# Kernel tuning notes

Measured on AMD Instinct MI355X. Metric: run time of the kernel, lower is better.

The kernel has to match this reference:

```python
import jax, jax.numpy as jnp
import numpy as np

N, E, IN, HID, H, C, L, G = 20000, 640000, 128, 256, 8, 32, 5, 64
NEG_SLOPE = 0.2


def _layernorm(x, g, b, eps=1e-5):
    mu = jnp.mean(x, axis=-1, keepdims=True)
    var = jnp.mean((x - mu) ** 2, axis=-1, keepdims=True)
    return (x - mu) * jax.lax.rsqrt(var + eps) * g + b


def _gatv2(h, src, dst, Wl, bl, Wr, br, att, out_bias):
    # h: [N, HID]; src/dst: [E+N] (self loops appended)
    n = h.shape[0]
    xl = (h @ Wl + bl).reshape(n, H, C)  # source transform
    xr = (h @ Wr + br).reshape(n, H, C)  # target transform
    e = jax.nn.leaky_relu(xl[src] + xr[dst], NEG_SLOPE)       # [Etot, H, C]
    logits = jnp.einsum('ehc,hc->eh', e, att)                  # [Etot, H]
    m = jax.ops.segment_max(logits, dst, num_segments=n)       # segment softmax over dst
    a = jnp.exp(logits - m[dst])
    s = jax.ops.segment_sum(a, dst, num_segments=n)
    alpha = a / (s[dst] + 1e-16)                               # [Etot, H]
    out = jax.ops.segment_sum(alpha[:, :, None] * xl[src], dst, num_segments=n)
    return out.reshape(n, HID) + out_bias


def setup_inputs() -> dict:
    key = jax.random.key(0)
    ks = jax.random.split(key, 16)
    sc = 0.05
    inp = {
        'x': jax.random.normal(ks[0], (N, IN), jnp.float32),
        'edge_index': jax.random.randint(ks[1], (2, E), 0, N, jnp.int64),
        'batch': jnp.sort(jax.random.randint(ks[2], (N,), 0, G, jnp.int64)),
        'proj_W': jax.random.normal(ks[3], (IN, HID), jnp.float32) * sc,
        'proj_b': jnp.zeros((HID,), jnp.float32),
        'Wl': jax.random.normal(ks[4], (L, HID, HID), jnp.float32) * sc,
        'bl': jnp.zeros((L, HID), jnp.float32),
        'Wr': jax.random.normal(ks[5], (L, HID, HID), jnp.float32) * sc,
        'br': jnp.zeros((L, HID), jnp.float32),
        'att': jax.random.normal(ks[6], (L, H, C), jnp.float32) * sc,
        'out_bias': jnp.zeros((L, HID), jnp.float32),
        'ln_g': jnp.ones((L, HID), jnp.float32),
        'ln_b': jnp.zeros((L, HID), jnp.float32),
    }
    return inp


def reference(x, edge_index, batch, proj_W, proj_b, Wl, bl, Wr, br, att, out_bias, ln_g, ln_b):
    n = x.shape[0]
    loops = jnp.arange(n, dtype=edge_index.dtype)
    src = jnp.concatenate([edge_index[0], loops])  # add_self_loops=True
    dst = jnp.concatenate([edge_index[1], loops])
    h = x @ proj_W + proj_b
    for i in range(L):  # dropout = identity in eval mode
        conv = _gatv2(h, src, dst, Wl[i], bl[i], Wr[i], br[i], att[i], out_bias[i])
        h = _layernorm(h + jax.nn.elu(conv), ln_g[i], ln_b[i])
    counts = jax.ops.segment_sum(jnp.ones((n,), h.dtype), batch, num_segments=G)
    gsum = jax.ops.segment_sum(h, batch, num_segments=G)
    graph_emb = gsum / jnp.maximum(counts, 1.0)[:, None]  # global_mean_pool
    return graph_emb, h, batch
```

## Files before the change

kernel.cpp:

```cpp
#include <hip/hip_runtime.h>
#include <hip/hip_bf16.h>

#define NN   20000
#define NE   640000
#define INF_ 128
#define HID  256
#define NL   5
#define NG   64

typedef __hip_bfloat16 bf16;
typedef __attribute__((ext_vector_type(4))) float f32x4;
typedef __attribute__((ext_vector_type(8))) short bf16x8;

#if __has_builtin(__builtin_amdgcn_exp2f)
#define EXP2F __builtin_amdgcn_exp2f
#else
#define EXP2F exp2f
#endif

__device__ __forceinline__ float b2f(bf16 v) { return __bfloat162float(v); }
__device__ __forceinline__ short f2bs(float v) {
  union { bf16 h; short s; } u; u.h = __float2bfloat16(v); return u.s;
}

#if __has_builtin(__builtin_amdgcn_update_dpp)
template<int CTRL>
__device__ __forceinline__ float dpp_add(float v) {
  int t = __builtin_amdgcn_update_dpp(0, __float_as_int(v), CTRL, 0xF, 0xF, true);
  return v + __int_as_float(t);
}
__device__ __forceinline__ float hsum8(float v) {
  v = dpp_add<0xB1>(v);
  v = dpp_add<0x4E>(v);
  v = dpp_add<0x141>(v);
  return v;
}
__device__ __forceinline__ float wsum64(float v) {
  v = hsum8(v);
  v = dpp_add<0x140>(v);
  v += __shfl_xor(v, 16);
  v += __shfl_xor(v, 32);
  return v;
}
#else
__device__ __forceinline__ float hsum8(float v) {
  v += __shfl_xor(v, 1);  v += __shfl_xor(v, 2);  v += __shfl_xor(v, 4);
  return v;
}
__device__ __forceinline__ float wsum64(float v) {
  v += __shfl_xor(v, 1);  v += __shfl_xor(v, 2);  v += __shfl_xor(v, 4);
  v += __shfl_xor(v, 8);  v += __shfl_xor(v, 16); v += __shfl_xor(v, 32);
  return v;
}
#endif

__global__ void detect_kernel(const int* __restrict__ ei,
                              const int* __restrict__ batch,
                              int* __restrict__ flags) {
  if (blockIdx.x == 0) {
    const int k = threadIdx.x;
    const bool e_bad = (k < 40) && (ei[2 * (k * 15999) + 1] != 0);
    const bool b_bad = (k < 40) && (batch[2 * (k * 249) + 1] != 0);
    const int e64 = __any(e_bad) ? 0 : 1;
    const int b64 = __any(b_bad) ? 0 : 1;
    if (k == 0) { flags[0] = e64; flags[1] = b64; }
  }
}

__device__ __forceinline__ int ld_i(const int* p, int f, size_t idx) {
  return f ? p[2 * idx] : p[idx];
}

__global__ void hist_kernel(const int* __restrict__ ei, const int* __restrict__ flags,
                            int* __restrict__ deg) {
  int e = blockIdx.x * blockDim.x + threadIdx.x;
  if (e >= NE) return;
  int f = flags[0];
  int d = ld_i(ei, f, (size_t)NE + e);
  if ((unsigned)d < NN) atomicAdd(&deg[d], 1);
}

#define SCAN_NB ((NN + 255) / 256)
__global__ __launch_bounds__(256) void scan1_kernel(
    const int* __restrict__ deg, int* __restrict__ off, int* __restrict__ bsum)
{
  __shared__ int sh[256];
  const int t = threadIdx.x;
  const int i = blockIdx.x * 256 + t;
  const int v = (i < NN) ? deg[i] : 0;
  sh[t] = v;
  __syncthreads();
  for (int d = 1; d < 256; d <<= 1) {
    int nv = (t >= d) ? sh[t - d] : 0;
    __syncthreads();
    sh[t] += nv;
    __syncthreads();
  }
  if (i < NN) off[i] = sh[t] - v;
  if (t == 255) bsum[blockIdx.x] = sh[255];
}

__global__ __launch_bounds__(128) void scan2_kernel(
    const int* __restrict__ bsum, int* __restrict__ boff, int* __restrict__ off)
{
  __shared__ int sh[128];
  const int t = threadIdx.x;
  const int v = (t < SCAN_NB) ? bsum[t] : 0;
  sh[t] = v;
  __syncthreads();
  for (int d = 1; d < 128; d <<= 1) {
    int nv = (t >= d) ? sh[t - d] : 0;
    __syncthreads();
    sh[t] += nv;
    __syncthreads();
  }
  if (t < SCAN_NB) boff[t] = sh[t] - v;
  if (t == SCAN_NB - 1) off[NN] = sh[t];
}

__global__ __launch_bounds__(256) void scan3_kernel(
    int* __restrict__ off, const int* __restrict__ boff, int* __restrict__ tmp)
{
  const int i = blockIdx.x * 256 + threadIdx.x;
  if (i < NN) {
    const int val = off[i] + boff[blockIdx.x];
    off[i] = val;
    tmp[i] = val;
  }
}

__global__ void scatter_kernel(const int* __restrict__ ei, const int* __restrict__ flags,
                               int* __restrict__ tmp, int* __restrict__ csr) {
  int e = blockIdx.x * blockDim.x + threadIdx.x;
  if (e >= NE) return;
  int f = flags[0];
  int d = ld_i(ei, f, (size_t)NE + e);
  int s = ld_i(ei, f, (size_t)e);
  if ((unsigned)d < NN) {
    int p = atomicAdd(&tmp[d], 1);
    int sv = ((unsigned)s < NN) ? s : 0;
    if ((unsigned)p < NE) csr[p] = sv * (HID * 2);
  }
}

__global__ __launch_bounds__(256) void prep_btf_kernel(
    const float* __restrict__ Wl, const float* __restrict__ Wr,
    short* __restrict__ BTl, short* __restrict__ BTr)
{
  const int z = blockIdx.y;
  const float* src = (z < NL) ? Wl + (size_t)z * HID * HID
                              : Wr + (size_t)(z - NL) * HID * HID;
  short* dst = (z < NL) ? BTl + (size_t)z * HID * HID
                        : BTr + (size_t)(z - NL) * HID * HID;
  const int g = blockIdx.x * 256 + threadIdx.x;
  const int ln   = g & 63;
  const int frag = (g >> 6) & 63;
  const int half = g >> 12;
  const int nf = frag >> 3, kk = frag & 7;
  const int n  = half * 128 + nf * 16 + (ln & 15);
  const int k0 = kk * 32 + (ln >> 4) * 8;
  bf16x8 outv;
#pragma unroll
  for (int j = 0; j < 8; ++j) outv[j] = f2bs(src[(size_t)(k0 + j) * HID + n]);
  *(bf16x8*)&dst[(size_t)g * 8] = outv;
}

template<int K, bool A_BF16>
__global__ __launch_bounds__(256) void gemm_bias_kernel(
    const void* __restrict__ Av, const float* __restrict__ B,
    const float* __restrict__ bias, float* __restrict__ Cf,
    bf16* __restrict__ Cb, int M)
{
  constexpr int N = 256;
  constexpr int LDB = K + 8;
  __shared__ __align__(16) short bT[32 * LDB];
  const int tid = threadIdx.x;
  const int n0 = blockIdx.x * 32;
  const int m_base = blockIdx.y * 256;

  if (tid < K) {
    const float* brow = B + (size_t)tid * N + n0;
#pragma unroll
    for (int j = 0; j < 32; ++j) bT[j * LDB + tid] = f2bs(brow[j]);
  }
  __syncthreads();

  const int wave = tid >> 6;
  const int lane = tid & 63;
  const int r    = lane & 15;
  const int quad = lane >> 4;
  const int m_wave = m_base + wave * 64;

  f32x4 acc[4][2];
#pragma unroll
  for (int i = 0; i < 4; ++i) { acc[i][0] = (f32x4)0.0f; acc[i][1] = (f32x4)0.0f; }

#pragma unroll
  for (int kk = 0; kk < K / 32; ++kk) {
    const int kof = kk * 32 + quad * 8;
    bf16x8 b0 = *(const bf16x8*)&bT[r * LDB + kof];
    bf16x8 b1 = *(const bf16x8*)&bT[(r + 16) * LDB + kof];
#pragma unroll
    for (int sm = 0; sm < 4; ++sm) {
      const int row = m_wave + sm * 16 + r;
      bf16x8 a = (bf16x8)(short)0;
      if (row < M) {
        if constexpr (A_BF16) {
          a = *(const bf16x8*)((const short*)Av + (size_t)row * K + kof);
        } else {
          const float* ap = (const float*)Av + (size_t)row * K + kof;
          f32x4 lo = *(const f32x4*)ap;
          f32x4 hi = *(const f32x4*)(ap + 4);
#pragma unroll
          for (int j = 0; j < 4; ++j) { a[j] = f2bs(lo[j]); a[4 + j] = f2bs(hi[j]); }
        }
      }
      acc[sm][0] = __builtin_amdgcn_mfma_f32_16x16x32_bf16(a, b0, acc[sm][0], 0, 0, 0);
      acc[sm][1] = __builtin_amdgcn_mfma_f32_16x16x32_bf16(a, b1, acc[sm][1], 0, 0, 0);
    }
  }

  const float bv0 = bias[n0 + r];
  const float bv1 = bias[n0 + 16 + r];
#pragma unroll
  for (int sm = 0; sm < 4; ++sm) {
#pragma unroll
    for (int rg = 0; rg < 4; ++rg) {
      const int row = m_wave + sm * 16 + quad * 4 + rg;
      if (row < M) {
        size_t i0 = (size_t)row * N + n0 + r;
        float v0 = acc[sm][0][rg] + bv0;
        float v1 = acc[sm][1][rg] + bv1;
        if (Cf) { Cf[i0] = v0; Cf[i0 + 16] = v1; }
        if (Cb) {
          ((unsigned short*)Cb)[i0]      = (unsigned short)f2bs(v0);
          ((unsigned short*)Cb)[i0 + 16] = (unsigned short)f2bs(v1);
        }
      }
    }
  }
}

template<bool A_BF16>
__global__ __launch_bounds__(256) void gemm_dual_kernel(
    const void* __restrict__ Av,
    const float* __restrict__ Bl, const float* __restrict__ Br,
    const float* __restrict__ bl, const float* __restrict__ br,
    bf16* __restrict__ Cl, bf16* __restrict__ Cr, int M)
{
  constexpr int K = HID, N = 256;
  constexpr int LDB = K + 8;
  __shared__ __align__(16) short bTl[32 * LDB];
  __shared__ __align__(16) short bTr[32 * LDB];
  const int tid = threadIdx.x;
  const int n0 = blockIdx.x * 32;
  const int m_base = blockIdx.y * 256;

  {
    const float* browl = Bl + (size_t)tid * N + n0;
    const float* browr = Br + (size_t)tid * N + n0;
#pragma unroll
    for (int j = 0; j < 32; ++j) {
      bTl[j * LDB + tid] = f2bs(browl[j]);
      bTr[j * LDB + tid] = f2bs(browr[j]);
    }
  }
  __syncthreads();

  const int wave = tid >> 6;
  const int lane = tid & 63;
  const int r    = lane & 15;
  const int quad = lane >> 4;
  const int m_wave = m_base + wave * 64;

  f32x4 accl[4][2], accr[4][2];
#pragma unroll
  for (int i = 0; i < 4; ++i) {
    accl[i][0] = (f32x4)0.0f; accl[i][1] = (f32x4)0.0f;
    accr[i][0] = (f32x4)0.0f; accr[i][1] = (f32x4)0.0f;
  }

#pragma unroll
  for (int kk = 0; kk < K / 32; ++kk) {
    const int kof = kk * 32 + quad * 8;
    bf16x8 b0l = *(const bf16x8*)&bTl[r * LDB + kof];
    bf16x8 b1l = *(const bf16x8*)&bTl[(r + 16) * LDB + kof];
    bf16x8 b0r = *(const bf16x8*)&bTr[r * LDB + kof];
    bf16x8 b1r = *(const bf16x8*)&bTr[(r + 16) * LDB + kof];
#pragma unroll
    for (int sm = 0; sm < 4; ++sm) {
      const int row = m_wave + sm * 16 + r;
      bf16x8 a = (bf16x8)(short)0;
      if (row < M) {
        if constexpr (A_BF16) {
          a = *(const bf16x8*)((const short*)Av + (size_t)row * K + kof);
        } else {
          const float* ap = (const float*)Av + (size_t)row * K + kof;
          f32x4 lo = *(const f32x4*)ap;
          f32x4 hi = *(const f32x4*)(ap + 4);
#pragma unroll
          for (int j = 0; j < 4; ++j) { a[j] = f2bs(lo[j]); a[4 + j] = f2bs(hi[j]); }
        }
      }
      accl[sm][0] = __builtin_amdgcn_mfma_f32_16x16x32_bf16(a, b0l, accl[sm][0], 0, 0, 0);
      accl[sm][1] = __builtin_amdgcn_mfma_f32_16x16x32_bf16(a, b1l, accl[sm][1], 0, 0, 0);
      accr[sm][0] = __builtin_amdgcn_mfma_f32_16x16x32_bf16(a, b0r, accr[sm][0], 0, 0, 0);
      accr[sm][1] = __builtin_amdgcn_mfma_f32_16x16x32_bf16(a, b1r, accr[sm][1], 0, 0, 0);
    }
  }

  const float bl0v = bl[n0 + r],  bl1v = bl[n0 + 16 + r];
  const float br0v = br[n0 + r],  br1v = br[n0 + 16 + r];
#pragma unroll
  for (int sm = 0; sm < 4; ++sm) {
#pragma unroll
    for (int rg = 0; rg < 4; ++rg) {
      const int row = m_wave + sm * 16 + quad * 4 + rg;
      if (row < M) {
        size_t i0 = (size_t)row * N + n0 + r;
        ((unsigned short*)Cl)[i0]      = (unsigned short)f2bs(accl[sm][0][rg] + bl0v);
        ((unsigned short*)Cl)[i0 + 16] = (unsigned short)f2bs(accl[sm][1][rg] + bl1v);
        ((unsigned short*)Cr)[i0]      = (unsigned short)f2bs(accr[sm][0][rg] + br0v);
        ((unsigned short*)Cr)[i0 + 16] = (unsigned short)f2bs(accr[sm][1][rg] + br1v);
      }
    }
  }
}

__global__ __launch_bounds__(256) void gemm_dual_tiled_kernel(
    const short* __restrict__ Ab,
    const short* __restrict__ BTl, const short* __restrict__ BTr,
    const float* __restrict__ bl, const float* __restrict__ br,
    bf16* __restrict__ Cl, bf16* __restrict__ Cr, int M)
{
  constexpr int K = HID;
  __shared__ __align__(16) short bfr[32768];
  const int tid  = threadIdx.x;
  const int lane = tid & 63;
  const int wv   = tid >> 6;
  const int bx   = blockIdx.x;
  const int n0   = (bx & 1) * 128;
  const short* BTf = (bx < 2) ? BTl : BTr;
  const float* bias = (bx < 2) ? bl : br;
  bf16* C = (bx < 2) ? Cl : Cr;
  const short* src = BTf + (size_t)(bx & 1) * 32768;

#pragma unroll
  for (int it = 0; it < 16; ++it) {
    const int c = it * 256 + tid;
    *(bf16x8*)&bfr[(size_t)c * 8] = *(const bf16x8*)&src[(size_t)c * 8];
  }

  const int r    = lane & 15;
  const int quad = lane >> 4;
  const int m_wave = blockIdx.y * 128 + wv * 32;

  const int ar0 = min(m_wave + r, M - 1);
  const int ar1 = min(m_wave + 16 + r, M - 1);
  const short* a0p = Ab + (size_t)ar0 * K + quad * 8;
  const short* a1p = Ab + (size_t)ar1 * K + quad * 8;
  bf16x8 a0[8], a1[8];
#pragma unroll
  for (int kk = 0; kk < 8; ++kk) {
    a0[kk] = *(const bf16x8*)(a0p + kk * 32);
    a1[kk] = *(const bf16x8*)(a1p + kk * 32);
  }

  __syncthreads();

  f32x4 acc[2][8];
#pragma unroll
  for (int sm = 0; sm < 2; ++sm)
#pragma unroll
    for (int nf = 0; nf < 8; ++nf) acc[sm][nf] = (f32x4)0.0f;

#pragma unroll
  for (int kk = 0; kk < 8; ++kk) {
#pragma unroll
    for (int nf = 0; nf < 8; ++nf) {
      const bf16x8 b = *(const bf16x8*)&bfr[((nf * 8 + kk) * 64 + lane) * 8];
      acc[0][nf] = __builtin_amdgcn_mfma_f32_16x16x32_bf16(a0[kk], b, acc[0][nf], 0, 0, 0);
      acc[1][nf] = __builtin_amdgcn_mfma_f32_16x16x32_bf16(a1[kk], b, acc[1][nf], 0, 0, 0);
    }
  }

  float bv[8];
#pragma unroll
  for (int nf = 0; nf < 8; ++nf) bv[nf] = bias[n0 + nf * 16 + r];

#pragma unroll
  for (int sm = 0; sm < 2; ++sm) {
#pragma unroll
    for (int rg = 0; rg < 4; ++rg) {
      const int row = m_wave + sm * 16 + quad * 4 + rg;
      if (row < M) {
        unsigned short* cp = (unsigned short*)C + (size_t)row * 256 + n0 + r;
#pragma unroll
        for (int nf = 0; nf < 8; ++nf)
          cp[nf * 16] = (unsigned short)f2bs(acc[sm][nf][rg] + bv[nf]);
      }
    }
  }
}

__global__ __launch_bounds__(256) void gat_layer_kernel(
    const bf16* __restrict__ xl, const bf16* __restrict__ xr,
    float* __restrict__ h, bf16* __restrict__ h_bf,
    const int* __restrict__ off, const int* __restrict__ csr,
    const float* __restrict__ att, const float* __restrict__ outb,
    const float* __restrict__ lng, const float* __restrict__ lnb)
{
  const int lane = threadIdx.x & 63;
  const int node = __builtin_amdgcn_readfirstlane(blockIdx.x * 4 + (threadIdx.x >> 6));
  const int cb   = ((lane >> 3) << 5) + ((lane & 7) << 2);
  const unsigned cb2  = (unsigned)cb * 2;
  const unsigned selfo = (unsigned)node * (HID * 2) + cb2;
  const size_t base = (size_t)node * HID + cb;
  const char* xlc = (const char*)xl;

  const uint2 uxr = *(const uint2*)((const char*)xr + selfo);
  const uint2 uxl = *(const uint2*)(xlc + selfo);
  f32x4 xrv, xls;
  xrv[0] = __uint_as_float(uxr.x << 16); xrv[1] = __uint_as_float(uxr.x & 0xffff0000u);
  xrv[2] = __uint_as_float(uxr.y << 16); xrv[3] = __uint_as_float(uxr.y & 0xffff0000u);
  xls[0] = __uint_as_float(uxl.x << 16); xls[1] = __uint_as_float(uxl.x & 0xffff0000u);
  xls[2] = __uint_as_float(uxl.y << 16); xls[3] = __uint_as_float(uxl.y & 0xffff0000u);

  const f32x4 av = *(const f32x4*)(att + cb);
  f32x4 a6, a4;
#pragma unroll
  for (int c = 0; c < 4; ++c) {
    a6[c] = av[c] * (0.6f * 1.44269504f);
    a4[c] = av[c] * (0.4f * 1.44269504f);
  }

  const f32x4 ob = *(const f32x4*)(outb + cb);
  const f32x4 hv = *(const f32x4*)(h + base);
  const f32x4 g4 = *(const f32x4*)(lng + cb);
  const f32x4 b4 = *(const f32x4*)(lnb + cb);

  float pa = 0.f;
#pragma unroll
  for (int c = 0; c < 4; ++c) {
    float z = xls[c] + xrv[c];
    pa = fmaf(a6[c], z, pa);
    pa = fmaf(a4[c], fabsf(z), pa);
  }
  const float es = EXP2F(hsum8(pa));
  float s = es;
  f32x4 o;
#pragma unroll
  for (int c = 0; c < 4; ++c) o[c] = es * xls[c];

  int beg = __builtin_amdgcn_readfirstlane(off[node]);
  int end = __builtin_amdgcn_readfirstlane(off[node + 1]);
  if (beg < 0) beg = 0;
  if (end > NE) end = NE;
  const unsigned* csrb = (const unsigned*)csr;

  const int nblk = (end > beg) ? ((end - beg) >> 3) : 0;

  unsigned adr[8];
  uint2 bufA[8], bufB[8];

  auto LOADADR = [&](int blk) {
    const int pp = beg + blk * 8;
#pragma unroll
    for (int j = 0; j < 8; ++j) adr[j] = csrb[pp + j];
  };
  auto GATHER = [&](uint2 (&buf)[8]) {
#pragma unroll
    for (int j = 0; j < 8; ++j) buf[j] = *(const uint2*)(xlc + (adr[j] + cb2));
  };
  auto COMPUTE = [&](const uint2 (&buf)[8]) {
    f32x4 xv[8];
#pragma unroll
    for (int j = 0; j < 8; ++j) {
      xv[j][0] = __uint_as_float(buf[j].x << 16);
      xv[j][1] = __uint_as_float(buf[j].x & 0xffff0000u);
      xv[j][2] = __uint_as_float(buf[j].y << 16);
      xv[j][3] = __uint_as_float(buf[j].y & 0xffff0000u);
    }
    float e[8];
#pragma unroll
    for (int j = 0; j < 8; ++j) {
      float acc = 0.f;
#pragma unroll
      for (int c = 0; c < 4; ++c) {
        float z = xv[j][c] + xrv[c];
        acc = fmaf(a6[c], z, acc);
        acc = fmaf(a4[c], fabsf(z), acc);
      }
      e[j] = EXP2F(hsum8(acc));
    }
    s += (((e[0] + e[1]) + (e[2] + e[3])) + ((e[4] + e[5]) + (e[6] + e[7])));
#pragma unroll
    for (int c = 0; c < 4; ++c) {
      float c0 = fmaf(e[0], xv[0][c], fmaf(e[1], xv[1][c],
                 fmaf(e[2], xv[2][c], fmaf(e[3], xv[3][c], o[c]))));
      float c1 = fmaf(e[4], xv[4][c], fmaf(e[5], xv[5][c],
                 fmaf(e[6], xv[6][c], e[7] * xv[7][c])));
      o[c] = c0 + c1;
    }
  };

  if (nblk > 0) {
    LOADADR(0);
    GATHER(bufA);
    if (nblk > 1) LOADADR(1);
  }
  int b = 0;
  for (; b + 2 <= nblk; b += 2) {
    GATHER(bufB);
    if (b + 2 < nblk) LOADADR(b + 2);
    COMPUTE(bufA);
    if (b + 2 < nblk) {
      GATHER(bufA);
      if (b + 3 < nblk) LOADADR(b + 3);
    }
    COMPUTE(bufB);
  }
  if (b < nblk) COMPUTE(bufA);

  for (int p = beg + nblk * 8; p < end; ++p) {
    const unsigned oo = csrb[p] + cb2;
    const uint2 u = *(const uint2*)(xlc + oo);
    f32x4 xv;
    xv[0] = __uint_as_float(u.x << 16); xv[1] = __uint_as_float(u.x & 0xffff0000u);
    xv[2] = __uint_as_float(u.y << 16); xv[3] = __uint_as_float(u.y & 0xffff0000u);
    float pe = 0.f;
#pragma unroll
    for (int c = 0; c < 4; ++c) {
      float z = xv[c] + xrv[c];
      pe = fmaf(a6[c], z, pe);
      pe = fmaf(a4[c], fabsf(z), pe);
    }
    const float ee = EXP2F(hsum8(pe));
    s += ee;
#pragma unroll
    for (int c = 0; c < 4; ++c) o[c] = fmaf(ee, xv[c], o[c]);
  }

  const float inv_s = 1.f / s;
  f32x4 res;
#pragma unroll
  for (int c = 0; c < 4; ++c) {
    float conv = fmaf(o[c], inv_s, ob[c]);
    float el = conv > 0.f ? conv : (__expf(conv) - 1.f);
    res[c] = hv[c] + el;
  }
  float pr = (res[0] + res[1]) + (res[2] + res[3]);
  const float mu = wsum64(pr) * (1.f / 256.f);
  f32x4 dv;
  float p2s = 0.f;
#pragma unroll
  for (int c = 0; c < 4; ++c) { dv[c] = res[c] - mu; p2s = fmaf(dv[c], dv[c], p2s); }
  const float var = wsum64(p2s) * (1.f / 256.f);
  const float rs = rsqrtf(var + 1e-5f);
  f32x4 y;
#pragma unroll
  for (int c = 0; c < 4; ++c) y[c] = fmaf(dv[c] * rs, g4[c], b4[c]);

  *(f32x4*)(h + base) = y;
  if (h_bf) {
    ushort4 u;
    u.x = (unsigned short)f2bs(y[0]);
    u.y = (unsigned short)f2bs(y[1]);
    u.z = (unsigned short)f2bs(y[2]);
    u.w = (unsigned short)f2bs(y[3]);
    *(ushort4*)((unsigned short*)h_bf + base) = u;
  }
}

__global__ __launch_bounds__(256) void pool_kernel(
    const float* __restrict__ h, const int* __restrict__ batch,
    const int* __restrict__ flags, float* __restrict__ gsum, int* __restrict__ gcnt)
{
  const int t = threadIdx.x;
  const int f = flags[1];
  int n0 = blockIdx.x * 80;
  int n1 = n0 + 80; if (n1 > NN) n1 = NN;
  float acc = 0.f;
  int g_cur = ld_i(batch, f, n0);
  if ((unsigned)g_cur >= NG) g_cur = 0;
  int run = 0;
  for (int n = n0; n < n1; ++n) {
    int g = ld_i(batch, f, n);
    if ((unsigned)g >= NG) g = 0;
    if (g != g_cur) {
      atomicAdd(&gsum[(size_t)g_cur * HID + t], acc);
      if (t == 0) atomicAdd(&gcnt[g_cur], run);
      acc = 0.f; run = 0; g_cur = g;
    }
    acc += h[(size_t)n * HID + t];
    ++run;
  }
  atomicAdd(&gsum[(size_t)g_cur * HID + t], acc);
  if (t == 0) atomicAdd(&gcnt[g_cur], run);
}

__global__ void write_out_kernel(const float* __restrict__ gsum, const int* __restrict__ gcnt,
                                 const int* __restrict__ batch,
                                 const int* __restrict__ flags, float* __restrict__ out)
{
  int i = blockIdx.x * blockDim.x + threadIdx.x;
  if (i < NG * HID) {
    int g = i >> 8;
    float c = (float)gcnt[g];
    c = c > 1.f ? c : 1.f;
    out[i] = gsum[i] / c;
  } else if (i < NG * HID + NN) {
    int n = i - NG * HID;
    int f = flags[1];
    out[(size_t)NG * HID + (size_t)NN * HID + n] = (float)ld_i(batch, f, (size_t)n);
  }
}

extern "C" void kernel_launch(void* const* d_in, const int* in_sizes, int n_in,
                              void* d_out, int out_size, void* d_ws, size_t ws_size,
                              hipStream_t stream) {
  (void)in_sizes; (void)n_in; (void)out_size;

  const float* x     = (const float*)d_in[0];
  const int*   ei    = (const int*)d_in[1];
  const int*   batch = (const int*)d_in[2];
  const float* projW = (const float*)d_in[3];
  const float* projB = (const float*)d_in[4];
  const float* Wl    = (const float*)d_in[5];
  const float* bl    = (const float*)d_in[6];
  const float* Wr    = (const float*)d_in[7];
  const float* br    = (const float*)d_in[8];
  const float* att   = (const float*)d_in[9];
  const float* outb  = (const float*)d_in[10];
  const float* lng   = (const float*)d_in[11];
  const float* lnb   = (const float*)d_in[12];
  float* out = (float*)d_out;

  float* h = out + (size_t)NG * HID;

  char* ws = (char*)d_ws;
  size_t o = 0;
  auto alloc = [&](size_t bytes) -> void* {
    void* p = ws + o;
    o += (bytes + 255) & ~(size_t)255;
    return p;
  };
  int*   flags = (int*)alloc(4 * 4);
  int*   deg   = (int*)alloc((size_t)NN * 4);
  int*   offs  = (int*)alloc((size_t)(NN + 1) * 4);
  int*   tmp   = (int*)alloc((size_t)NN * 4);
  float* gsum  = (float*)alloc((size_t)NG * HID * 4);
  int*   gcnt  = (int*)alloc((size_t)NG * 4);
  int*   bsum  = (int*)alloc((size_t)(SCAN_NB + 1) * 4);
  int*   boff  = (int*)alloc((size_t)(SCAN_NB + 1) * 4);
  int*   csr   = (int*)alloc((size_t)NE * 4);
  bf16*  xl    = (bf16*)alloc((size_t)NN * HID * 2);
  bf16*  xr    = (bf16*)alloc((size_t)NN * HID * 2);
  size_t o_base = o;
  bf16*  h_bf  = (bf16*)alloc((size_t)NN * HID * 2);
  const bool use_hbf = (ws_size >= o);
  if (!use_hbf) { h_bf = nullptr; o = o_base; }
  size_t o_hbf = o;
  short* BTl = (short*)alloc((size_t)NL * HID * HID * 2);
  short* BTr = (short*)alloc((size_t)NL * HID * HID * 2);
  const bool use_bt = use_hbf && (ws_size >= o);
  if (!use_bt) { o = o_hbf; }

  hipMemsetAsync(deg, 0, (size_t)NN * 4, stream);
  hipMemsetAsync(gsum, 0, (size_t)NG * HID * 4 + (size_t)NG * 4, stream);

  detect_kernel<<<1, 64, 0, stream>>>(ei, batch, flags);

  if (use_bt) {
    dim3 pg(32, 2 * NL);
    prep_btf_kernel<<<pg, 256, 0, stream>>>(Wl, Wr, BTl, BTr);
  }

  hist_kernel<<<(NE + 255) / 256, 256, 0, stream>>>(ei, flags, deg);
  scan1_kernel<<<SCAN_NB, 256, 0, stream>>>(deg, offs, bsum);
  scan2_kernel<<<1, 128, 0, stream>>>(bsum, boff, offs);
  scan3_kernel<<<SCAN_NB, 256, 0, stream>>>(offs, boff, tmp);
  scatter_kernel<<<(NE + 255) / 256, 256, 0, stream>>>(ei, flags, tmp, csr);

  dim3 gg(HID / 32, (NN + 255) / 256);

  gemm_bias_kernel<INF_, false><<<gg, 256, 0, stream>>>(x, projW, projB, h, h_bf, NN);

  dim3 gt(4, (NN + 127) / 128);
  for (int i = 0; i < NL; ++i) {
    if (use_bt) {
      gemm_dual_tiled_kernel<<<gt, 256, 0, stream>>>((const short*)h_bf,
          BTl + (size_t)i * HID * HID, BTr + (size_t)i * HID * HID,
          bl + (size_t)i * HID, br + (size_t)i * HID, xl, xr, NN);
    } else if (use_hbf) {
      gemm_dual_kernel<true><<<gg, 256, 0, stream>>>(h_bf,
          Wl + (size_t)i * HID * HID, Wr + (size_t)i * HID * HID,
          bl + (size_t)i * HID, br + (size_t)i * HID, xl, xr, NN);
    } else {
      gemm_dual_kernel<false><<<gg, 256, 0, stream>>>(h,
          Wl + (size_t)i * HID * HID, Wr + (size_t)i * HID * HID,
          bl + (size_t)i * HID, br + (size_t)i * HID, xl, xr, NN);
    }
    gat_layer_kernel<<<NN / 4, 256, 0, stream>>>(xl, xr, h, h_bf, offs, csr,
                                                 att + (size_t)i * HID, outb + (size_t)i * HID,
                                                 lng + (size_t)i * HID, lnb + (size_t)i * HID);
  }

  pool_kernel<<<250, 256, 0, stream>>>(h, batch, flags, gsum, gcnt);
  write_out_kernel<<<(NG * HID + NN + 255) / 256, 256, 0, stream>>>(gsum, gcnt, batch, flags, out);
}
```

Before: 523.4 us.

## Use pre-packed bf16 MFMA tiled GEMM for input projection; simplify gather pipeline

Adds kernels that convert x to bf16 and pre-pack projW into MFMA fragment layout, then runs the input projection with a tiled MFMA kernel instead of the generic GEMM that transposes B into shared memory per block. Separately, the GAT layer gather loop drops the double-buffered A/B scheme for a single buffer that prefetches only the next block's CSR addresses. This adds two small prep kernels and extra workspace use. The simpler gather loop may expose more memory latency but uses fewer registers.

```diff
diff --git a/kernel.cpp b/kernel.cpp
--- a/kernel.cpp
+++ b/kernel.cpp
@@ -21,6 +21,15 @@
 __device__ __forceinline__ float b2f(bf16 v) { return __bfloat162float(v); }
 __device__ __forceinline__ short f2bs(float v) {
   union { bf16 h; short s; } u; u.h = __float2bfloat16(v); return u.s;
+}
+__device__ __forceinline__ f32x4 ldbf4o(const char* __restrict__ basep, unsigned off) {
+  const uint2 u = *(const uint2*)(basep + off);
+  f32x4 r;
+  r[0] = __uint_as_float(u.x << 16);
+  r[1] = __uint_as_float(u.x & 0xffff0000u);
+  r[2] = __uint_as_float(u.y << 16);
+  r[3] = __uint_as_float(u.y & 0xffff0000u);
+  return r;
 }
 
 #if __has_builtin(__builtin_amdgcn_update_dpp)
@@ -141,6 +150,20 @@
     int sv = ((unsigned)s < NN) ? s : 0;
     if ((unsigned)p < NE) csr[p] = sv * (HID * 2);
   }
+}
+
+__global__ __launch_bounds__(256) void xbf_kernel(
+    const float* __restrict__ x, short* __restrict__ x_bf)
+{
+  const int i = blockIdx.x * 256 + threadIdx.x;
+  if (i >= NN * INF_ / 8) return;
+  const float* s = x + (size_t)i * 8;
+  f32x4 lo = *(const f32x4*)s;
+  f32x4 hi = *(const f32x4*)(s + 4);
+  bf16x8 v;
+#pragma unroll
+  for (int j = 0; j < 4; ++j) { v[j] = f2bs(lo[j]); v[4 + j] = f2bs(hi[j]); }
+  *(bf16x8*)&x_bf[(size_t)i * 8] = v;
 }
 
 __global__ __launch_bounds__(256) void prep_btf_kernel(
@@ -165,6 +188,22 @@
   *(bf16x8*)&dst[(size_t)g * 8] = outv;
 }
 
+__global__ __launch_bounds__(256) void prep_btfp_kernel(
+    const float* __restrict__ projW, short* __restrict__ BTp)
+{
+  const int g = blockIdx.x * 256 + threadIdx.x;
+  const int ln   = g & 63;
+  const int frag = (g >> 6) & 31;
+  const int half = g >> 11;
+  const int nf = frag >> 2, kk = frag & 3;
+  const int n  = half * 128 + nf * 16 + (ln & 15);
+  const int k0 = kk * 32 + (ln >> 4) * 8;
+  bf16x8 outv;
+#pragma unroll
+  for (int j = 0; j < 8; ++j) outv[j] = f2bs(projW[(size_t)(k0 + j) * HID + n]);
+  *(bf16x8*)&BTp[(size_t)g * 8] = outv;
+}
+
 template<int K, bool A_BF16>
 __global__ __launch_bounds__(256) void gemm_bias_kernel(
     const void* __restrict__ Av, const float* __restrict__ B,
@@ -403,6 +442,82 @@
   }
 }
 
+__global__ __launch_bounds__(256) void gemm_proj_tiled_kernel(
+    const short* __restrict__ Ax,
+    const short* __restrict__ BTp,
+    const float* __restrict__ bias, float* __restrict__ Cf,
+    bf16* __restrict__ Cb, int M)
+{
+  constexpr int K = INF_;
+  __shared__ __align__(16) short bfr[16384];
+  const int tid  = threadIdx.x;
+  const int lane = tid & 63;
+  const int wv   = tid >> 6;
+  const int bx   = blockIdx.x;
+  const int n0   = bx * 128;
+  const short* src = BTp + (size_t)bx * 16384;
+
+#pragma unroll
+  for (int it = 0; it < 8; ++it) {
+    const int c = it * 256 + tid;
+    *(bf16x8*)&bfr[(size_t)c * 8] = *(const bf16x8*)&src[(size_t)c * 8];
+  }
+
+  const int r    = lane & 15;
+  const int quad = lane >> 4;
+  const int m_wave = blockIdx.y * 128 + wv * 32;
+
+  const int ar0 = min(m_wave + r, M - 1);
+  const int ar1 = min(m_wave + 16 + r, M - 1);
+  const short* a0p = Ax + (size_t)ar0 * K + quad * 8;
+  const short* a1p = Ax + (size_t)ar1 * K + quad * 8;
+  bf16x8 a0[4], a1[4];
+#pragma unroll
+  for (int kk = 0; kk < 4; ++kk) {
+    a0[kk] = *(const bf16x8*)(a0p + kk * 32);
+    a1[kk] = *(const bf16x8*)(a1p + kk * 32);
+  }
+
+  __syncthreads();
+
+  f32x4 acc[2][8];
+#pragma unroll
+  for (int sm = 0; sm < 2; ++sm)
+#pragma unroll
+    for (int nf = 0; nf < 8; ++nf) acc[sm][nf] = (f32x4)0.0f;
+
+#pragma unroll
+  for (int kk = 0; kk < 4; ++kk) {
+#pragma unroll
+    for (int nf = 0; nf < 8; ++nf) {
+      const bf16x8 b = *(const bf16x8*)&bfr[((nf * 4 + kk) * 64 + lane) * 8];
+      acc[0][nf] = __builtin_amdgcn_mfma_f32_16x16x32_bf16(a0[kk], b, acc[0][nf], 0, 0, 0);
+      acc[1][nf] = __builtin_amdgcn_mfma_f32_16x16x32_bf16(a1[kk], b, acc[1][nf], 0, 0, 0);
+    }
+  }
+
+  float bv[8];
+#pragma unroll
+  for (int nf = 0; nf < 8; ++nf) bv[nf] = bias[n0 + nf * 16 + r];
+
+#pragma unroll
+  for (int sm = 0; sm < 2; ++sm) {
+#pragma unroll
+    for (int rg = 0; rg < 4; ++rg) {
+      const int row = m_wave + sm * 16 + quad * 4 + rg;
+      if (row < M) {
+        const size_t i0 = (size_t)row * 256 + n0 + r;
+#pragma unroll
+        for (int nf = 0; nf < 8; ++nf) {
+          const float v = acc[sm][nf][rg] + bv[nf];
+          Cf[i0 + nf * 16] = v;
+          ((unsigned short*)Cb)[i0 + nf * 16] = (unsigned short)f2bs(v);
+        }
+      }
+    }
+  }
+}
+
 __global__ __launch_bounds__(256) void gat_layer_kernel(
     const bf16* __restrict__ xl, const bf16* __restrict__ xr,
     float* __restrict__ h, bf16* __restrict__ h_bf,
@@ -418,14 +533,8 @@
   const size_t base = (size_t)node * HID + cb;
   const char* xlc = (const char*)xl;
 
-  const uint2 uxr = *(const uint2*)((const char*)xr + selfo);
-  const uint2 uxl = *(const uint2*)(xlc + selfo);
-  f32x4 xrv, xls;
-  xrv[0] = __uint_as_float(uxr.x << 16); xrv[1] = __uint_as_float(uxr.x & 0xffff0000u);
-  xrv[2] = __uint_as_float(uxr.y << 16); xrv[3] = __uint_as_float(uxr.y & 0xffff0000u);
-  xls[0] = __uint_as_float(uxl.x << 16); xls[1] = __uint_as_float(uxl.x & 0xffff0000u);
-  xls[2] = __uint_as_float(uxl.y << 16); xls[3] = __uint_as_float(uxl.y & 0xffff0000u);
-
+  const f32x4 xrv = ldbf4o((const char*)xr, selfo);
+  const f32x4 xls = ldbf4o(xlc, selfo);
   const f32x4 av = *(const f32x4*)(att + cb);
   f32x4 a6, a4;
 #pragma unroll
@@ -459,27 +568,19 @@
   const unsigned* csrb = (const unsigned*)csr;
 
   const int nblk = (end > beg) ? ((end - beg) >> 3) : 0;
-
-  unsigned adr[8];
-  uint2 bufA[8], bufB[8];
-
-  auto LOADADR = [&](int blk) {
-    const int pp = beg + blk * 8;
-#pragma unroll
-    for (int j = 0; j < 8; ++j) adr[j] = csrb[pp + j];
-  };
-  auto GATHER = [&](uint2 (&buf)[8]) {
-#pragma unroll
-    for (int j = 0; j < 8; ++j) buf[j] = *(const uint2*)(xlc + (adr[j] + cb2));
-  };
-  auto COMPUTE = [&](const uint2 (&buf)[8]) {
+  unsigned nx[8];
+  if (nblk > 0) {
+#pragma unroll
+    for (int j = 0; j < 8; ++j) nx[j] = csrb[beg + j];
+  }
+  for (int b = 0; b < nblk; ++b) {
     f32x4 xv[8];
 #pragma unroll
-    for (int j = 0; j < 8; ++j) {
-      xv[j][0] = __uint_as_float(buf[j].x << 16);
-      xv[j][1] = __uint_as_float(buf[j].x & 0xffff0000u);
-      xv[j][2] = __uint_as_float(buf[j].y << 16);
-      xv[j][3] = __uint_as_float(buf[j].y & 0xffff0000u);
+    for (int j = 0; j < 8; ++j) xv[j] = ldbf4o(xlc, nx[j] + cb2);
+    if (b + 1 < nblk) {
+      const int pn = beg + (b + 1) * 8;
+#pragma unroll
+      for (int j = 0; j < 8; ++j) nx[j] = csrb[pn + j];
     }
     float e[8];
 #pragma unroll
@@ -502,32 +603,10 @@
                  fmaf(e[6], xv[6][c], e[7] * xv[7][c])));
       o[c] = c0 + c1;
     }
-  };
-
-  if (nblk > 0) {
-    LOADADR(0);
-    GATHER(bufA);
-    if (nblk > 1) LOADADR(1);
-  }
-  int b = 0;
-  for (; b + 2 <= nblk; b += 2) {
-    GATHER(bufB);
-    if (b + 2 < nblk) LOADADR(b + 2);
-    COMPUTE(bufA);
-    if (b + 2 < nblk) {
-      GATHER(bufA);
-      if (b + 3 < nblk) LOADADR(b + 3);
-    }
-    COMPUTE(bufB);
-  }
-  if (b < nblk) COMPUTE(bufA);
-
+  }
   for (int p = beg + nblk * 8; p < end; ++p) {
     const unsigned oo = csrb[p] + cb2;
-    const uint2 u = *(const uint2*)(xlc + oo);
-    f32x4 xv;
-    xv[0] = __uint_as_float(u.x << 16); xv[1] = __uint_as_float(u.x & 0xffff0000u);
-    xv[2] = __uint_as_float(u.y << 16); xv[3] = __uint_as_float(u.y & 0xffff0000u);
+    const f32x4 xv = ldbf4o(xlc, oo);
     float pe = 0.f;
 #pragma unroll
     for (int c = 0; c < 4; ++c) {
@@ -665,6 +744,11 @@
   short* BTr = (short*)alloc((size_t)NL * HID * HID * 2);
   const bool use_bt = use_hbf && (ws_size >= o);
   if (!use_bt) { o = o_hbf; }
+  size_t o_bt = o;
+  short* x_bf = (short*)alloc((size_t)NN * INF_ * 2);
+  short* BTp  = (short*)alloc((size_t)HID * INF_ * 2);
+  const bool use_xbf = use_bt && (ws_size >= o);
+  if (!use_xbf) { o = o_bt; }
 
   hipMemsetAsync(deg, 0, (size_t)NN * 4, stream);
   hipMemsetAsync(gsum, 0, (size_t)NG * HID * 4 + (size_t)NG * 4, stream);
@@ -674,6 +758,10 @@
   if (use_bt) {
     dim3 pg(32, 2 * NL);
     prep_btf_kernel<<<pg, 256, 0, stream>>>(Wl, Wr, BTl, BTr);
+  }
+  if (use_xbf) {
+    prep_btfp_kernel<<<16, 256, 0, stream>>>(projW, BTp);
+    xbf_kernel<<<(NN * INF_ / 8 + 255) / 256, 256, 0, stream>>>(x, x_bf);
   }
 
   hist_kernel<<<(NE + 255) / 256, 256, 0, stream>>>(ei, flags, deg);
@@ -684,7 +772,12 @@
 
   dim3 gg(HID / 32, (NN + 255) / 256);
 
-  gemm_bias_kernel<INF_, false><<<gg, 256, 0, stream>>>(x, projW, projB, h, h_bf, NN);
+  if (use_xbf) {
+    dim3 gp(2, (NN + 127) / 128);
+    gemm_proj_tiled_kernel<<<gp, 256, 0, stream>>>(x_bf, BTp, projB, h, h_bf, NN);
+  } else {
+    gemm_bias_kernel<INF_, false><<<gg, 256, 0, stream>>>(x, projW, projB, h, h_bf, NN);
+  }
 
   dim3 gt(4, (NN + 127) / 128);
   for (int i = 0; i < NL; ++i) {
```

Result: faster. 509.1 us (-2.7%).
